# Performance work log

Measured on AMD Instinct MI355X. Metric: run time of the kernel, lower is better.

Reference implementation:

```python
import jax, jax.numpy as jnp
import numpy as np
import math

CHANNELS = 512
OUT_CHANNELS = 512
N_HEADS = 8
WINDOW = 4
K_CH = CHANNELS // N_HEADS


def _conv1x1(x, W, b):
    # x: (B, C_in, T), W: (C_out, C_in), b: (C_out,)
    return jnp.einsum('oc,bct->bot', W, x) + b[None, :, None]


def _get_relative_embeddings(emb, length, window=WINDOW):
    # emb: (H, 2*window+1, k_ch) -> (H, 2*length-1, k_ch)
    pad_length = max(length - (window + 1), 0)
    start = max(window + 1 - length, 0)
    e = jnp.pad(emb, ((0, 0), (pad_length, pad_length), (0, 0))) if pad_length > 0 else emb
    return e[:, start:start + 2 * length - 1]


def _relative_to_absolute(x):
    # x: (B, H, L, 2L-1) -> (B, H, L, L)
    b, h, L, _ = x.shape
    x = jnp.pad(x, ((0, 0), (0, 0), (0, 0), (0, 1)))          # (B,H,L,2L)
    xf = x.reshape(b, h, L * 2 * L)
    xf = jnp.pad(xf, ((0, 0), (0, 0), (L - 1, 0)))
    return xf.reshape(b, h, L + 1, 2 * L - 1)[:, :, :L, L - 1:]


def _absolute_to_relative(x):
    # x: (B, H, L, L) -> (B, H, L, 2L-1)
    b, h, L, _ = x.shape
    x = jnp.pad(x, ((0, 0), (0, 0), (0, 0), (0, L - 1)))       # (B,H,L,2L-1)
    xf = x.reshape(b, h, L * (2 * L - 1))
    xf = jnp.pad(xf, ((0, 0), (0, 0), (L, 0)))
    return xf.reshape(b, h, L, 2 * L)[:, :, :, 1:]


def setup_inputs() -> dict:
    key = jax.random.key(0)
    ks = jax.random.split(key, 16)
    B, C, T = 4, CHANNELS, 1024
    xavier = math.sqrt(2.0 / (C + C))
    rel_std = K_CH ** -0.5
    return {
        'x_q': jax.random.normal(ks[0], (B, C, T), jnp.float32),
        'x_k': jax.random.normal(ks[1], (B, C, T), jnp.float32),
        'x_v': jax.random.normal(ks[2], (B, C, T), jnp.float32),
        'Wq': jax.random.normal(ks[3], (C, C), jnp.float32) * xavier,
        'bq': jnp.zeros((C,), jnp.float32),
        'Wk': jax.random.normal(ks[4], (C, C), jnp.float32) * xavier,
        'bk': jnp.zeros((C,), jnp.float32),
        'Wv': jax.random.normal(ks[5], (C, C), jnp.float32) * xavier,
        'bv': jnp.zeros((C,), jnp.float32),
        'Wo': jax.random.normal(ks[6], (OUT_CHANNELS, C), jnp.float32) * xavier,
        'bo': jnp.zeros((OUT_CHANNELS,), jnp.float32),
        'emb_rel_k': jax.random.normal(ks[7], (N_HEADS, 2 * WINDOW + 1, K_CH), jnp.float32) * rel_std,
        'emb_rel_v': jax.random.normal(ks[8], (N_HEADS, 2 * WINDOW + 1, K_CH), jnp.float32) * rel_std,
    }


def reference(x_q, x_k, x_v, Wq, bq, Wk, bk, Wv, bv, Wo, bo, emb_rel_k, emb_rel_v):
    q = _conv1x1(x_q, Wq, bq)
    k = _conv1x1(x_k, Wk, bk)
    v = _conv1x1(x_v, Wv, bv)
    B, C, T = q.shape
    # (B, C, T) -> (B, H, T, k_ch); head h owns contiguous k_ch channel chunk
    qh = q.reshape(B, N_HEADS, K_CH, T).transpose(0, 1, 3, 2) / math.sqrt(K_CH)
    kh = k.reshape(B, N_HEADS, K_CH, T).transpose(0, 1, 3, 2)
    vh = v.reshape(B, N_HEADS, K_CH, T).transpose(0, 1, 3, 2)
    scores = jnp.einsum('bhtd,bhsd->bhts', qh, kh)              # (B,H,T,T)
    rel_k = _get_relative_embeddings(emb_rel_k, T)              # (H,2T-1,d)
    rel_logits = jnp.einsum('bhtd,hmd->bhtm', qh, rel_k)        # (B,H,T,2T-1)
    scores = scores + _relative_to_absolute(rel_logits)
    attn = jax.nn.softmax(scores, axis=-1)
    ctx = jnp.einsum('bhts,bhsd->bhtd', attn, vh)
    rel_w = _absolute_to_relative(attn)                         # (B,H,T,2T-1)
    rel_v = _get_relative_embeddings(emb_rel_v, T)
    ctx = ctx + jnp.einsum('bhtm,hmd->bhtd', rel_w, rel_v)
    out = ctx.transpose(0, 1, 3, 2).reshape(B, C, T)
    return _conv1x1(out, Wo, bo)
```

## Files before the change

### kernel.cpp

```cpp
#include <hip/hip_runtime.h>

#define T_LEN 1024
#define NH 8
#define DH 64
#define CCH 512
#define LOG2E 1.44269504088896340736f

typedef _Float16 f16;
typedef _Float16 f16x8 __attribute__((ext_vector_type(8)));
typedef _Float16 f16x4 __attribute__((ext_vector_type(4)));
typedef float f32x4 __attribute__((ext_vector_type(4)));

__device__ __forceinline__ void dma16(const void* g, void* l)
{
    __builtin_amdgcn_global_load_lds((const __attribute__((address_space(1))) void*)g,
                                     (__attribute__((address_space(3))) void*)l, 16, 0, 0);
}

__global__ __launch_bounds__(256)
void prep_kernel(const float* __restrict__ x0, const float* __restrict__ x1,
                 const float* __restrict__ x2, const float* __restrict__ W0,
                 const float* __restrict__ W1, const float* __restrict__ W2,
                 const float* __restrict__ W3, f16* __restrict__ o0,
                 f16* __restrict__ o1, f16* __restrict__ o2, f16* __restrict__ w0,
                 f16* __restrict__ w1, f16* __restrict__ w2, f16* __restrict__ w3,
                 int B)
{
    const int z = blockIdx.z;
    if (z < 3 * B) {
        const int t0 = blockIdx.x * 64, c0 = blockIdx.y * 64;
        const int which = z / B, b = z % B;
        const float* x = (which == 0) ? x0 : (which == 1) ? x1 : x2;
        f16* o = (which == 0) ? o0 : (which == 1) ? o1 : o2;

        __shared__ float L[64 * 68];
        const int cl = threadIdx.x & 63, g = threadIdx.x >> 6;
        const float* src = x + ((size_t)(b * CCH + c0 + cl)) * T_LEN + t0 + g * 16;
        #pragma unroll
        for (int j = 0; j < 4; ++j)
            *(float4*)&L[cl * 68 + g * 16 + 4 * j] = *(const float4*)&src[4 * j];
        __syncthreads();
        const int tl = threadIdx.x & 63, cg = (threadIdx.x >> 6) * 16;
        f16 h[16];
        #pragma unroll
        for (int j = 0; j < 16; ++j) h[j] = (f16)L[(cg + j) * 68 + tl];
        f16* dst = o + ((size_t)(b * T_LEN + t0 + tl)) * CCH + c0 + cg;
        *(f16x8*)&dst[0] = *(f16x8*)&h[0];
        *(f16x8*)&dst[8] = *(f16x8*)&h[8];
    } else {
        const int slice = z - 3 * B;
        size_t i = ((size_t)(slice * 128 + blockIdx.y * 16 + blockIdx.x) * 256 + threadIdx.x) * 4;
        const int wi = (int)(i >> 18);
        const size_t off = i & 262143;
        const float* src = (wi == 0) ? W0 : (wi == 1) ? W1 : (wi == 2) ? W2 : W3;
        f16* dst = (wi == 0) ? w0 : (wi == 1) ? w1 : (wi == 2) ? w2 : w3;
        float4 v4 = *(const float4*)&src[off];
        f16x4 h = {(f16)v4.x, (f16)v4.y, (f16)v4.z, (f16)v4.w};
        *(f16x4*)&dst[off] = h;
    }
}

__global__ __launch_bounds__(256)
void proj_qkv(const f16* __restrict__ xq, const f16* __restrict__ xk,
              const f16* __restrict__ xv, const f16* __restrict__ wq,
              const f16* __restrict__ wk, const f16* __restrict__ wv,
              const float* __restrict__ bq, const float* __restrict__ bk,
              const float* __restrict__ bv, f16* __restrict__ qo,
              f16* __restrict__ ko, f16* __restrict__ vo)
{
    const int which = blockIdx.z;
    const f16* X = (which == 0) ? xq : (which == 1) ? xk : xv;
    const f16* W = (which == 0) ? wq : (which == 1) ? wk : wv;
    const float* bias = (which == 0) ? bq : (which == 1) ? bk : bv;
    const float scale = (which == 0) ? 0.125f * LOG2E : 1.0f;

    const int r0 = blockIdx.x * 128;
    const int o0 = blockIdx.y * 64;
    const int tid = threadIdx.x;
    const int w = tid >> 6, lane = tid & 63;
    const int quad = lane >> 4, l15 = lane & 15;

    __shared__ __align__(16) f16 Xs[2][128 * 64];
    __shared__ __align__(16) f16 Ws[2][64 * 64];

    const int srow = tid >> 3;
    const int scol = ((tid & 7) ^ (srow & 7)) << 3;

    const f16* Xg = X + (size_t)(r0 + srow) * CCH + scol;
    const f16* Wg = W + (size_t)(o0 + srow) * CCH + scol;

    #pragma unroll
    for (int j = 0; j < 4; ++j)
        dma16(Xg + (size_t)(32 * j) * CCH, &Xs[0][(size_t)tid * 8 + j * 2048]);
    #pragma unroll
    for (int j = 0; j < 2; ++j)
        dma16(Wg + (size_t)(32 * j) * CCH, &Ws[0][(size_t)tid * 8 + j * 2048]);

    f32x4 acc[8] = {};

    for (int kc = 0; kc < 8; ++kc) {
        __syncthreads();
        if (kc < 7) {
            const int bf = (kc + 1) & 1, c1 = (kc + 1) * 64;
            #pragma unroll
            for (int j = 0; j < 4; ++j)
                dma16(Xg + c1 + (size_t)(32 * j) * CCH, &Xs[bf][(size_t)tid * 8 + j * 2048]);
            #pragma unroll
            for (int j = 0; j < 2; ++j)
                dma16(Wg + c1 + (size_t)(32 * j) * CCH, &Ws[bf][(size_t)tid * 8 + j * 2048]);
        }
        const int cb = kc & 1;
        #pragma unroll
        for (int ks = 0; ks < 2; ++ks) {
            const int sl = ((ks * 4 + quad) ^ (l15 & 7)) << 3;
            f16x8 xf[2], wf[4];
            #pragma unroll
            for (int im = 0; im < 2; ++im)
                xf[im] = *(const f16x8*)&Xs[cb][(32 * w + 16 * im + l15) * 64 + sl];
            #pragma unroll
            for (int cm = 0; cm < 4; ++cm)
                wf[cm] = *(const f16x8*)&Ws[cb][(16 * cm + l15) * 64 + sl];
            if (which < 2) {
                #pragma unroll
                for (int im = 0; im < 2; ++im)
                    #pragma unroll
                    for (int cm = 0; cm < 4; ++cm)
                        acc[im * 4 + cm] = __builtin_amdgcn_mfma_f32_16x16x32_f16(
                            xf[im], wf[cm], acc[im * 4 + cm], 0, 0, 0);
            } else {
                #pragma unroll
                for (int cm = 0; cm < 4; ++cm)
                    #pragma unroll
                    for (int in = 0; in < 2; ++in)
                        acc[cm * 2 + in] = __builtin_amdgcn_mfma_f32_16x16x32_f16(
                            wf[cm], xf[in], acc[cm * 2 + in], 0, 0, 0);
            }
        }
    }

    if (which < 2) {
        f16* out = (which == 0) ? qo : ko;
        float bl[4];
        #pragma unroll
        for (int cm = 0; cm < 4; ++cm) bl[cm] = bias[o0 + 16 * cm + l15];
        #pragma unroll
        for (int im = 0; im < 2; ++im)
            #pragma unroll
            for (int r = 0; r < 4; ++r) {
                size_t row = (size_t)(r0 + 32 * w + 16 * im + 4 * quad + r) * CCH;
                #pragma unroll
                for (int cm = 0; cm < 4; ++cm)
                    out[row + o0 + 16 * cm + l15] =
                        (f16)((acc[im * 4 + cm][r] + bl[cm]) * scale);
            }
    } else {
        const int bb = r0 >> 10, tb = r0 & 1023;
        #pragma unroll
        for (int cm = 0; cm < 4; ++cm) {
            float4 bv4 = *(const float4*)&bias[o0 + 16 * cm + 4 * quad];
            float bl[4] = {bv4.x, bv4.y, bv4.z, bv4.w};
            #pragma unroll
            for (int r = 0; r < 4; ++r) {
                size_t row = ((size_t)(bb * CCH + o0 + 16 * cm + 4 * quad + r)) * T_LEN;
                #pragma unroll
                for (int in = 0; in < 2; ++in)
                    vo[row + tb + 32 * w + 16 * in + l15] =
                        (f16)(acc[cm * 2 + in][r] + bl[r]);
            }
        }
    }
}

__global__ __launch_bounds__(256)
void attn_mfma(const f16* __restrict__ q, const f16* __restrict__ kk,
               const f16* __restrict__ v, const float* __restrict__ ekg,
               const float* __restrict__ evg, f16* __restrict__ Op0,
               f16* __restrict__ Op1, float* __restrict__ l0,
               float* __restrict__ l1)
{
    const int t0 = blockIdx.x * 64, h = blockIdx.y;
    const int b = blockIdx.z >> 1, split = blockIdx.z & 1;
    const int tid = threadIdx.x;
    const int w = tid >> 6, lane = tid & 63;
    const int quad = lane >> 4, l15 = lane & 15;

    f16* Op = split ? Op1 : Op0;
    float* lbuf = split ? l1 : l0;

    __shared__ __align__(16) f16 Qs[4096], Ks[4096], Vs[4096], Ps[4096];
    __shared__ float eks[576], evs[576];

    const int srow = tid >> 3;
    const int scol = ((tid & 7) ^ (srow & 7)) << 3;

    for (int i = tid; i < 576; i += 256) {
        eks[i] = ekg[h * 576 + i];
        evs[i] = evg[h * 576 + i];
    }

    dma16(q + ((size_t)(b * T_LEN + t0 + srow)) * CCH + h * DH + scol, &Qs[(size_t)tid * 8]);
    dma16(q + ((size_t)(b * T_LEN + t0 + srow + 32)) * CCH + h * DH + scol, &Qs[((size_t)tid + 256) * 8]);
    __syncthreads();

    f16x8 qf[2];
    #pragma unroll
    for (int ks = 0; ks < 2; ++ks)
        qf[ks] = *(const f16x8*)&Qs[(16 * w + l15) * 64 + (((ks * 4 + quad) ^ (l15 & 7)) << 3)];

    const int kb0 = split * 8;
    const f16* gk = kk + ((size_t)(b * T_LEN + kb0 * 64 + srow)) * CCH + h * DH + scol;
    const f16* gv = v + ((size_t)(b * CCH + h * DH + srow)) * T_LEN + kb0 * 64 + scol;

    const int myt = 16 * w + l15;
    float Ssum = 0.f;
    f32x4 O[4] = {};

    const bool corner_hi = (blockIdx.x == 0) && (split == 1);
    const bool corner_lo = (blockIdx.x == 15) && (split == 0);

    for (int kb = kb0; kb < kb0 + 8; ++kb) {
        __syncthreads();
        dma16(gk, &Ks[(size_t)tid * 8]);
        dma16(gk + (size_t)32 * CCH, &Ks[((size_t)tid + 256) * 8]);
        dma16(gv, &Vs[(size_t)tid * 8]);
        dma16(gv + (size_t)32 * T_LEN, &Vs[((size_t)tid + 256) * 8]);
        gk += (size_t)64 * CCH;
        gv += 64;
        __syncthreads();

        f32x4 S[4] = {};
        #pragma unroll
        for (int ks = 0; ks < 2; ++ks) {
            #pragma unroll
            for (int ct = 0; ct < 4; ++ct) {
                f16x8 a = *(const f16x8*)&Ks[(16 * ct + l15) * 64 + (((ks * 4 + quad) ^ (l15 & 7)) << 3)];
                S[ct] = __builtin_amdgcn_mfma_f32_16x16x32_f16(a, qf[ks], S[ct], 0, 0, 0);
            }
        }

        if ((corner_hi && kb == 15) || (corner_lo && kb == 0)) {
            const int s0g = kb * 64;
            #pragma unroll
            for (int ct = 0; ct < 4; ++ct)
                #pragma unroll
                for (int r = 0; r < 4; ++r) {
                    int t_g = t0 + myt;
                    int s_g = s0g + 16 * ct + 4 * quad + r;
                    int df = s_g - t_g;
                    if (df >= 1019 && df <= 1023) {
                        const float* ekp = &eks[(df - 1019) * 64];
                        float sacc = 0.f;
                        for (int d = 0; d < 64; ++d)
                            sacc += (float)Qs[myt * 64 + (((d >> 3) ^ (myt & 7)) << 3) + (d & 7)] * ekp[d];
                        S[ct][r] += sacc;
                    } else if (df >= -1023 && df <= -1021) {
                        const float* ekp = &eks[(1029 + df) * 64];
                        const int t2 = myt - 1;
                        float sacc = 0.f;
                        for (int d = 0; d < 64; ++d)
                            sacc += (float)Qs[t2 * 64 + (((d >> 3) ^ (t2 & 7)) << 3) + (d & 7)] * ekp[d];
                        S[ct][r] += sacc;
                    }
                }
        }

        #pragma unroll
        for (int ct = 0; ct < 4; ++ct) {
            f16x4 pk_;
            #pragma unroll
            for (int r = 0; r < 4; ++r) {
                float p = exp2f(S[ct][r]);
                Ssum += p;
                pk_[r] = (f16)p;
            }
            int colh = (((2 * ct + (quad >> 1)) ^ (myt & 7)) << 3) + (quad & 1) * 4;
            *(f16x4*)&Ps[myt * 64 + colh] = pk_;
        }
        __syncthreads();

        #pragma unroll
        for (int ks = 0; ks < 2; ++ks) {
            f16x8 a = *(const f16x8*)&Ps[(16 * w + l15) * 64 + (((ks * 4 + quad) ^ (l15 & 7)) << 3)];
            #pragma unroll
            for (int ct = 0; ct < 4; ++ct) {
                f16x8 bf = *(const f16x8*)&Vs[(16 * ct + l15) * 64 + (((ks * 4 + quad) ^ (l15 & 7)) << 3)];
                O[ct] = __builtin_amdgcn_mfma_f32_16x16x32_f16(a, bf, O[ct], 0, 0, 0);
            }
        }

        const int s0g = kb * 64;
        if (s0g <= t0 + 67 && s0g + 63 >= t0 - 4) {
            #pragma unroll
            for (int r = 0; r < 4; ++r) {
                int t_loc = 16 * w + 4 * quad + r;
                int t_g = t0 + t_loc;
                int slo = max(s0g, t_g - 4), shi = min(s0g + 63, t_g + 4);
                for (int s = slo; s <= shi; ++s) {
                    int sl = s - s0g;
                    float p = (float)Ps[t_loc * 64 + (((sl >> 3) ^ (t_loc & 7)) << 3) + (sl & 7)];
                    const float* evp = &evs[(s - t_g + 4) * 64];
                    #pragma unroll
                    for (int ct = 0; ct < 4; ++ct)
                        O[ct][r] += p * evp[16 * ct + l15];
                }
            }
        }
    }

    Ssum += __shfl_xor(Ssum, 16);
    Ssum += __shfl_xor(Ssum, 32);
    if (quad == 0)
        lbuf[((size_t)b * NH + h) * T_LEN + t0 + myt] = Ssum;

    #pragma unroll
    for (int r = 0; r < 4; ++r) {
        int t_g = t0 + 16 * w + 4 * quad + r;
        size_t rowo = ((size_t)(b * T_LEN + t_g)) * CCH + h * DH;
        #pragma unroll
        for (int ct = 0; ct < 4; ++ct)
            Op[rowo + 16 * ct + l15] = (f16)O[ct][r];
    }
}

__global__ __launch_bounds__(256)
void combine_kernel(const f16* __restrict__ Op0, const f16* __restrict__ Op1,
                    const float* __restrict__ l0, const float* __restrict__ l1,
                    f16* __restrict__ ctx)
{
    const size_t i8 = ((size_t)blockIdx.x * 256 + threadIdx.x) * 8;
    const size_t gr = i8 >> 9;
    const int h = (int)((i8 & 511) >> 6);
    const size_t li = ((gr >> 10) * NH + h) * T_LEN + (gr & 1023);
    const float rl = 1.0f / (l0[li] + l1[li]);
    f16x8 a0 = *(const f16x8*)&Op0[i8];
    f16x8 a1 = *(const f16x8*)&Op1[i8];
    f16 o[8];
    #pragma unroll
    for (int e = 0; e < 8; ++e)
        o[e] = (f16)(((float)a0[e] + (float)a1[e]) * rl);
    *(f16x8*)&ctx[i8] = *(f16x8*)o;
}

__global__ __launch_bounds__(256)
void proj_out(const f16* __restrict__ ctx, const f16* __restrict__ Wo,
              const float* __restrict__ bo, float* __restrict__ out)
{
    const int r0 = blockIdx.x * 128;
    const int o0 = blockIdx.y * 64;
    const int tid = threadIdx.x;
    const int w = tid >> 6, lane = tid & 63;
    const int quad = lane >> 4, l15 = lane & 15;

    __shared__ __align__(16) f16 Cs[2][128 * 64];
    __shared__ __align__(16) f16 Ws[2][64 * 64];

    const int srow = tid >> 3;
    const int scol = ((tid & 7) ^ (srow & 7)) << 3;

    const f16* Cg = ctx + (size_t)(r0 + srow) * CCH + scol;
    const f16* Wg = Wo + (size_t)(o0 + srow) * CCH + scol;

    #pragma unroll
    for (int j = 0; j < 4; ++j)
        dma16(Cg + (size_t)(32 * j) * CCH, &Cs[0][(size_t)tid * 8 + j * 2048]);
    #pragma unroll
    for (int j = 0; j < 2; ++j)
        dma16(Wg + (size_t)(32 * j) * CCH, &Ws[0][(size_t)tid * 8 + j * 2048]);

    f32x4 acc[8] = {};

    for (int kc = 0; kc < 8; ++kc) {
        __syncthreads();
        if (kc < 7) {
            const int bf = (kc + 1) & 1, c1 = (kc + 1) * 64;
            #pragma unroll
            for (int j = 0; j < 4; ++j)
                dma16(Cg + c1 + (size_t)(32 * j) * CCH, &Cs[bf][(size_t)tid * 8 + j * 2048]);
            #pragma unroll
            for (int j = 0; j < 2; ++j)
                dma16(Wg + c1 + (size_t)(32 * j) * CCH, &Ws[bf][(size_t)tid * 8 + j * 2048]);
        }
        const int cb = kc & 1;
        #pragma unroll
        for (int ks = 0; ks < 2; ++ks) {
            const int sl = ((ks * 4 + quad) ^ (l15 & 7)) << 3;
            f16x8 cf[2], wf[4];
            #pragma unroll
            for (int in = 0; in < 2; ++in)
                cf[in] = *(const f16x8*)&Cs[cb][(32 * w + 16 * in + l15) * 64 + sl];
            #pragma unroll
            for (int cm = 0; cm < 4; ++cm)
                wf[cm] = *(const f16x8*)&Ws[cb][(16 * cm + l15) * 64 + sl];
            #pragma unroll
            for (int cm = 0; cm < 4; ++cm)
                #pragma unroll
                for (int in = 0; in < 2; ++in)
                    acc[cm * 2 + in] = __builtin_amdgcn_mfma_f32_16x16x32_f16(
                        wf[cm], cf[in], acc[cm * 2 + in], 0, 0, 0);
        }
    }

    const int bb = r0 >> 10, tb = r0 & 1023;
    #pragma unroll
    for (int cm = 0; cm < 4; ++cm) {
        float4 bv4 = *(const float4*)&bo[o0 + 16 * cm + 4 * quad];
        float bl[4] = {bv4.x, bv4.y, bv4.z, bv4.w};
        #pragma unroll
        for (int r = 0; r < 4; ++r) {
            size_t row = ((size_t)(bb * CCH + o0 + 16 * cm + 4 * quad + r)) * T_LEN;
            #pragma unroll
            for (int in = 0; in < 2; ++in)
                out[row + tb + 32 * w + 16 * in + l15] = acc[cm * 2 + in][r] + bl[r];
        }
    }
}

extern "C" void kernel_launch(void* const* d_in, const int* in_sizes, int n_in,
                              void* d_out, int out_size, void* d_ws, size_t ws_size,
                              hipStream_t stream)
{
    const float* x_q = (const float*)d_in[0];
    const float* x_k = (const float*)d_in[1];
    const float* x_v = (const float*)d_in[2];
    const float* Wq  = (const float*)d_in[3];
    const float* bq  = (const float*)d_in[4];
    const float* Wk  = (const float*)d_in[5];
    const float* bk  = (const float*)d_in[6];
    const float* Wv  = (const float*)d_in[7];
    const float* bv  = (const float*)d_in[8];
    const float* Wo  = (const float*)d_in[9];
    const float* bo  = (const float*)d_in[10];
    const float* erk = (const float*)d_in[11];
    const float* erv = (const float*)d_in[12];

    const int B = in_sizes[0] / (CCH * T_LEN);
    const size_t te = (size_t)B * CCH * T_LEN;
    const size_t we = (size_t)CCH * CCH;

    f16* p = (f16*)d_ws;
    f16* xTq = p; p += te;
    f16* xTk = p; p += te;
    f16* xTv = p; p += te;
    f16* wqh = p; p += we;
    f16* wkh = p; p += we;
    f16* wvh = p; p += we;
    f16* woh = p; p += we;
    f16* qh  = p; p += te;
    f16* kh  = p; p += te;
    f16* vh  = p; p += te;
    f16* Op0 = p; p += te;
    f16* Op1 = p; p += te;
    f16* ch  = p; p += te;
    float* l0 = (float*)p;
    float* l1 = l0 + (size_t)B * NH * T_LEN;

    dim3 blk(256);
    prep_kernel<<<dim3(16, 8, 3 * B + 8), blk, 0, stream>>>(
        x_q, x_k, x_v, Wq, Wk, Wv, Wo, xTq, xTk, xTv, wqh, wkh, wvh, woh, B);
    proj_qkv<<<dim3(B * 8, 8, 3), blk, 0, stream>>>(
        xTq, xTk, xTv, wqh, wkh, wvh, bq, bk, bv, qh, kh, vh);
    attn_mfma<<<dim3(T_LEN / 64, NH, 2 * B), blk, 0, stream>>>(
        qh, kh, vh, erk, erv, Op0, Op1, l0, l1);
    combine_kernel<<<dim3(B * 256), blk, 0, stream>>>(Op0, Op1, l0, l1, ch);
    proj_out<<<dim3(B * 8, 8), blk, 0, stream>>>(ch, woh, bo, (float*)d_out);
}
```

Before: 159.8 us.

## Load unshared MFMA operands directly from global memory instead of LDS

In the QKV projection, attention and output projection kernels, operand tiles that each wave uses alone (X rows, K and V tiles, context rows) are no longer staged through shared memory. Each lane now reads its MFMA fragment straight from global memory, which removes DMA copies, LDS traffic and two barriers per key block in attention. The output projection also halves its row tile to 64 so there are twice as many blocks. The cost is uncoalesced 16-byte global reads that depend on cache hits, and K/V loads that are no longer prefetched.

```diff
diff --git a/kernel.cpp b/kernel.cpp
--- a/kernel.cpp
+++ b/kernel.cpp
@@ -80,18 +80,14 @@
     const int w = tid >> 6, lane = tid & 63;
     const int quad = lane >> 4, l15 = lane & 15;
 
-    __shared__ __align__(16) f16 Xs[2][128 * 64];
     __shared__ __align__(16) f16 Ws[2][64 * 64];
 
     const int srow = tid >> 3;
     const int scol = ((tid & 7) ^ (srow & 7)) << 3;
-
-    const f16* Xg = X + (size_t)(r0 + srow) * CCH + scol;
     const f16* Wg = W + (size_t)(o0 + srow) * CCH + scol;
 
-    #pragma unroll
-    for (int j = 0; j < 4; ++j)
-        dma16(Xg + (size_t)(32 * j) * CCH, &Xs[0][(size_t)tid * 8 + j * 2048]);
+    const f16* xp = X + (size_t)(r0 + 32 * w + l15) * CCH + quad * 8;
+
     #pragma unroll
     for (int j = 0; j < 2; ++j)
         dma16(Wg + (size_t)(32 * j) * CCH, &Ws[0][(size_t)tid * 8 + j * 2048]);
@@ -103,9 +99,6 @@
         if (kc < 7) {
             const int bf = (kc + 1) & 1, c1 = (kc + 1) * 64;
             #pragma unroll
-            for (int j = 0; j < 4; ++j)
-                dma16(Xg + c1 + (size_t)(32 * j) * CCH, &Xs[bf][(size_t)tid * 8 + j * 2048]);
-            #pragma unroll
             for (int j = 0; j < 2; ++j)
                 dma16(Wg + c1 + (size_t)(32 * j) * CCH, &Ws[bf][(size_t)tid * 8 + j * 2048]);
         }
@@ -116,7 +109,7 @@
             f16x8 xf[2], wf[4];
             #pragma unroll
             for (int im = 0; im < 2; ++im)
-                xf[im] = *(const f16x8*)&Xs[cb][(32 * w + 16 * im + l15) * 64 + sl];
+                xf[im] = *(const f16x8*)&xp[(size_t)(16 * im) * CCH + kc * 64 + ks * 32];
             #pragma unroll
             for (int cm = 0; cm < 4; ++cm)
                 wf[cm] = *(const f16x8*)&Ws[cb][(16 * cm + l15) * 64 + sl];
@@ -187,7 +180,7 @@
     f16* Op = split ? Op1 : Op0;
     float* lbuf = split ? l1 : l0;
 
-    __shared__ __align__(16) f16 Qs[4096], Ks[4096], Vs[4096], Ps[4096];
+    __shared__ __align__(16) f16 Qs[4096], Ps[4096];
     __shared__ float eks[576], evs[576];
 
     const int srow = tid >> 3;
@@ -208,8 +201,8 @@
         qf[ks] = *(const f16x8*)&Qs[(16 * w + l15) * 64 + (((ks * 4 + quad) ^ (l15 & 7)) << 3)];
 
     const int kb0 = split * 8;
-    const f16* gk = kk + ((size_t)(b * T_LEN + kb0 * 64 + srow)) * CCH + h * DH + scol;
-    const f16* gv = v + ((size_t)(b * CCH + h * DH + srow)) * T_LEN + kb0 * 64 + scol;
+    const f16* kp = kk + ((size_t)(b * T_LEN + kb0 * 64 + l15)) * CCH + h * DH + quad * 8;
+    const f16* vp = v + ((size_t)(b * CCH + h * DH + l15)) * T_LEN + kb0 * 64 + quad * 8;
 
     const int myt = 16 * w + l15;
     float Ssum = 0.f;
@@ -219,23 +212,18 @@
     const bool corner_lo = (blockIdx.x == 15) && (split == 0);
 
     for (int kb = kb0; kb < kb0 + 8; ++kb) {
-        __syncthreads();
-        dma16(gk, &Ks[(size_t)tid * 8]);
-        dma16(gk + (size_t)32 * CCH, &Ks[((size_t)tid + 256) * 8]);
-        dma16(gv, &Vs[(size_t)tid * 8]);
-        dma16(gv + (size_t)32 * T_LEN, &Vs[((size_t)tid + 256) * 8]);
-        gk += (size_t)64 * CCH;
-        gv += 64;
-        __syncthreads();
+        const int ko = (kb - kb0) * 64;
 
         f32x4 S[4] = {};
         #pragma unroll
         for (int ks = 0; ks < 2; ++ks) {
-            #pragma unroll
-            for (int ct = 0; ct < 4; ++ct) {
-                f16x8 a = *(const f16x8*)&Ks[(16 * ct + l15) * 64 + (((ks * 4 + quad) ^ (l15 & 7)) << 3)];
-                S[ct] = __builtin_amdgcn_mfma_f32_16x16x32_f16(a, qf[ks], S[ct], 0, 0, 0);
-            }
+            f16x8 kf[4];
+            #pragma unroll
+            for (int ct = 0; ct < 4; ++ct)
+                kf[ct] = *(const f16x8*)&kp[(size_t)(ko + 16 * ct) * CCH + ks * 32];
+            #pragma unroll
+            for (int ct = 0; ct < 4; ++ct)
+                S[ct] = __builtin_amdgcn_mfma_f32_16x16x32_f16(kf[ct], qf[ks], S[ct], 0, 0, 0);
         }
 
         if ((corner_hi && kb == 15) || (corner_lo && kb == 0)) {
@@ -264,28 +252,34 @@
                 }
         }
 
-        #pragma unroll
-        for (int ct = 0; ct < 4; ++ct) {
-            f16x4 pk_;
+        f16x4 pk_[4];
+        #pragma unroll
+        for (int ct = 0; ct < 4; ++ct)
             #pragma unroll
             for (int r = 0; r < 4; ++r) {
                 float p = exp2f(S[ct][r]);
                 Ssum += p;
-                pk_[r] = (f16)p;
-            }
+                pk_[ct][r] = (f16)p;
+            }
+
+        __syncthreads();
+        #pragma unroll
+        for (int ct = 0; ct < 4; ++ct) {
             int colh = (((2 * ct + (quad >> 1)) ^ (myt & 7)) << 3) + (quad & 1) * 4;
-            *(f16x4*)&Ps[myt * 64 + colh] = pk_;
+            *(f16x4*)&Ps[myt * 64 + colh] = pk_[ct];
         }
         __syncthreads();
 
         #pragma unroll
         for (int ks = 0; ks < 2; ++ks) {
             f16x8 a = *(const f16x8*)&Ps[(16 * w + l15) * 64 + (((ks * 4 + quad) ^ (l15 & 7)) << 3)];
-            #pragma unroll
-            for (int ct = 0; ct < 4; ++ct) {
-                f16x8 bf = *(const f16x8*)&Vs[(16 * ct + l15) * 64 + (((ks * 4 + quad) ^ (l15 & 7)) << 3)];
-                O[ct] = __builtin_amdgcn_mfma_f32_16x16x32_f16(a, bf, O[ct], 0, 0, 0);
-            }
+            f16x8 vf[4];
+            #pragma unroll
+            for (int ct = 0; ct < 4; ++ct)
+                vf[ct] = *(const f16x8*)&vp[(size_t)(16 * ct) * T_LEN + ko + ks * 32];
+            #pragma unroll
+            for (int ct = 0; ct < 4; ++ct)
+                O[ct] = __builtin_amdgcn_mfma_f32_16x16x32_f16(a, vf[ct], O[ct], 0, 0, 0);
         }
 
         const int s0g = kb * 64;
@@ -345,38 +339,31 @@
 void proj_out(const f16* __restrict__ ctx, const f16* __restrict__ Wo,
               const float* __restrict__ bo, float* __restrict__ out)
 {
-    const int r0 = blockIdx.x * 128;
+    const int r0 = blockIdx.x * 64;
     const int o0 = blockIdx.y * 64;
     const int tid = threadIdx.x;
     const int w = tid >> 6, lane = tid & 63;
     const int quad = lane >> 4, l15 = lane & 15;
 
-    __shared__ __align__(16) f16 Cs[2][128 * 64];
     __shared__ __align__(16) f16 Ws[2][64 * 64];
 
     const int srow = tid >> 3;
     const int scol = ((tid & 7) ^ (srow & 7)) << 3;
-
-    const f16* Cg = ctx + (size_t)(r0 + srow) * CCH + scol;
     const f16* Wg = Wo + (size_t)(o0 + srow) * CCH + scol;
 
-    #pragma unroll
-    for (int j = 0; j < 4; ++j)
-        dma16(Cg + (size_t)(32 * j) * CCH, &Cs[0][(size_t)tid * 8 + j * 2048]);
+    const f16* cp = ctx + (size_t)(r0 + 16 * w + l15) * CCH + quad * 8;
+
     #pragma unroll
     for (int j = 0; j < 2; ++j)
         dma16(Wg + (size_t)(32 * j) * CCH, &Ws[0][(size_t)tid * 8 + j * 2048]);
 
-    f32x4 acc[8] = {};
+    f32x4 acc[4] = {};
 
     for (int kc = 0; kc < 8; ++kc) {
         __syncthreads();
         if (kc < 7) {
             const int bf = (kc + 1) & 1, c1 = (kc + 1) * 64;
             #pragma unroll
-            for (int j = 0; j < 4; ++j)
-                dma16(Cg + c1 + (size_t)(32 * j) * CCH, &Cs[bf][(size_t)tid * 8 + j * 2048]);
-            #pragma unroll
             for (int j = 0; j < 2; ++j)
                 dma16(Wg + c1 + (size_t)(32 * j) * CCH, &Ws[bf][(size_t)tid * 8 + j * 2048]);
         }
@@ -384,19 +371,12 @@
         #pragma unroll
         for (int ks = 0; ks < 2; ++ks) {
             const int sl = ((ks * 4 + quad) ^ (l15 & 7)) << 3;
-            f16x8 cf[2], wf[4];
-            #pragma unroll
-            for (int in = 0; in < 2; ++in)
-                cf[in] = *(const f16x8*)&Cs[cb][(32 * w + 16 * in + l15) * 64 + sl];
-            #pragma unroll
-            for (int cm = 0; cm < 4; ++cm)
-                wf[cm] = *(const f16x8*)&Ws[cb][(16 * cm + l15) * 64 + sl];
-            #pragma unroll
-            for (int cm = 0; cm < 4; ++cm)
-                #pragma unroll
-                for (int in = 0; in < 2; ++in)
-                    acc[cm * 2 + in] = __builtin_amdgcn_mfma_f32_16x16x32_f16(
-                        wf[cm], cf[in], acc[cm * 2 + in], 0, 0, 0);
+            f16x8 cf = *(const f16x8*)&cp[kc * 64 + ks * 32];
+            #pragma unroll
+            for (int cm = 0; cm < 4; ++cm) {
+                f16x8 wf = *(const f16x8*)&Ws[cb][(16 * cm + l15) * 64 + sl];
+                acc[cm] = __builtin_amdgcn_mfma_f32_16x16x32_f16(wf, cf, acc[cm], 0, 0, 0);
+            }
         }
     }
 
@@ -408,9 +388,7 @@
         #pragma unroll
         for (int r = 0; r < 4; ++r) {
             size_t row = ((size_t)(bb * CCH + o0 + 16 * cm + 4 * quad + r)) * T_LEN;
-            #pragma unroll
-            for (int in = 0; in < 2; ++in)
-                out[row + tb + 32 * w + 16 * in + l15] = acc[cm * 2 + in][r] + bl[r];
+            out[row + tb + 16 * w + l15] = acc[cm][r] + bl[r];
         }
     }
 }
@@ -462,5 +440,5 @@
     attn_mfma<<<dim3(T_LEN / 64, NH, 2 * B), blk, 0, stream>>>(
         qh, kh, vh, erk, erv, Op0, Op1, l0, l1);
     combine_kernel<<<dim3(B * 256), blk, 0, stream>>>(Op0, Op1, l0, l1, ch);
-    proj_out<<<dim3(B * 8, 8), blk, 0, stream>>>(ch, woh, bo, (float*)d_out);
-}
+    proj_out<<<dim3(B * 16, 8), blk, 0, stream>>>(ch, woh, bo, (float*)d_out);
+}
```

After: 213.4 us. +33.5%, slower.

## Double-buffer K/V tiles in attention and fuse split-combine into output projection

Applied to the files above, without the earlier changes.

The attention kernel now keeps two K/V shared-memory buffers and issues the next tile's loads after the softmax barrier, so they overlap with the PV MFMA work instead of stalling at the top of each iteration. The separate combine kernel is removed. Its normalization of the two split partial outputs moves into proj_out's tile loading, which reads both partials, scales by the reciprocal row sums from shared memory, and writes f16 into LDS. This saves a launch and the ctx round trip through memory. In exchange, proj_out uses register-staged loads instead of async LDS DMA and rereads the partials once per output-column block, and the attention kernel uses more LDS.

```diff
diff --git a/kernel.cpp b/kernel.cpp
--- a/kernel.cpp
+++ b/kernel.cpp
@@ -187,7 +187,8 @@
     f16* Op = split ? Op1 : Op0;
     float* lbuf = split ? l1 : l0;
 
-    __shared__ __align__(16) f16 Qs[4096], Ks[4096], Vs[4096], Ps[4096];
+    __shared__ __align__(16) f16 Qs[4096], Ps[4096];
+    __shared__ __align__(16) f16 Ks[2][4096], Vs[2][4096];
     __shared__ float eks[576], evs[576];
 
     const int srow = tid >> 3;
@@ -198,19 +199,23 @@
         evs[i] = evg[h * 576 + i];
     }
 
-    dma16(q + ((size_t)(b * T_LEN + t0 + srow)) * CCH + h * DH + scol, &Qs[(size_t)tid * 8]);
-    dma16(q + ((size_t)(b * T_LEN + t0 + srow + 32)) * CCH + h * DH + scol, &Qs[((size_t)tid + 256) * 8]);
-    __syncthreads();
-
-    f16x8 qf[2];
-    #pragma unroll
-    for (int ks = 0; ks < 2; ++ks)
-        qf[ks] = *(const f16x8*)&Qs[(16 * w + l15) * 64 + (((ks * 4 + quad) ^ (l15 & 7)) << 3)];
-
     const int kb0 = split * 8;
     const f16* gk = kk + ((size_t)(b * T_LEN + kb0 * 64 + srow)) * CCH + h * DH + scol;
     const f16* gv = v + ((size_t)(b * CCH + h * DH + srow)) * T_LEN + kb0 * 64 + scol;
 
+    dma16(q + ((size_t)(b * T_LEN + t0 + srow)) * CCH + h * DH + scol, &Qs[(size_t)tid * 8]);
+    dma16(q + ((size_t)(b * T_LEN + t0 + srow + 32)) * CCH + h * DH + scol, &Qs[((size_t)tid + 256) * 8]);
+    dma16(gk, &Ks[0][(size_t)tid * 8]);
+    dma16(gk + (size_t)32 * CCH, &Ks[0][((size_t)tid + 256) * 8]);
+    dma16(gv, &Vs[0][(size_t)tid * 8]);
+    dma16(gv + (size_t)32 * T_LEN, &Vs[0][((size_t)tid + 256) * 8]);
+    __syncthreads();
+
+    f16x8 qf[2];
+    #pragma unroll
+    for (int ks = 0; ks < 2; ++ks)
+        qf[ks] = *(const f16x8*)&Qs[(16 * w + l15) * 64 + (((ks * 4 + quad) ^ (l15 & 7)) << 3)];
+
     const int myt = 16 * w + l15;
     float Ssum = 0.f;
     f32x4 O[4] = {};
@@ -218,22 +223,16 @@
     const bool corner_hi = (blockIdx.x == 0) && (split == 1);
     const bool corner_lo = (blockIdx.x == 15) && (split == 0);
 
-    for (int kb = kb0; kb < kb0 + 8; ++kb) {
-        __syncthreads();
-        dma16(gk, &Ks[(size_t)tid * 8]);
-        dma16(gk + (size_t)32 * CCH, &Ks[((size_t)tid + 256) * 8]);
-        dma16(gv, &Vs[(size_t)tid * 8]);
-        dma16(gv + (size_t)32 * T_LEN, &Vs[((size_t)tid + 256) * 8]);
-        gk += (size_t)64 * CCH;
-        gv += 64;
-        __syncthreads();
+    for (int it = 0; it < 8; ++it) {
+        const int kb = kb0 + it, cb = it & 1;
+        if (it) __syncthreads();
 
         f32x4 S[4] = {};
         #pragma unroll
         for (int ks = 0; ks < 2; ++ks) {
             #pragma unroll
             for (int ct = 0; ct < 4; ++ct) {
-                f16x8 a = *(const f16x8*)&Ks[(16 * ct + l15) * 64 + (((ks * 4 + quad) ^ (l15 & 7)) << 3)];
+                f16x8 a = *(const f16x8*)&Ks[cb][(16 * ct + l15) * 64 + (((ks * 4 + quad) ^ (l15 & 7)) << 3)];
                 S[ct] = __builtin_amdgcn_mfma_f32_16x16x32_f16(a, qf[ks], S[ct], 0, 0, 0);
             }
         }
@@ -278,12 +277,20 @@
         }
         __syncthreads();
 
+        if (it < 7) {
+            const int nb = cb ^ 1;
+            dma16(gk + (size_t)((it + 1) * 64) * CCH, &Ks[nb][(size_t)tid * 8]);
+            dma16(gk + (size_t)((it + 1) * 64 + 32) * CCH, &Ks[nb][((size_t)tid + 256) * 8]);
+            dma16(gv + (it + 1) * 64, &Vs[nb][(size_t)tid * 8]);
+            dma16(gv + (size_t)32 * T_LEN + (it + 1) * 64, &Vs[nb][((size_t)tid + 256) * 8]);
+        }
+
         #pragma unroll
         for (int ks = 0; ks < 2; ++ks) {
             f16x8 a = *(const f16x8*)&Ps[(16 * w + l15) * 64 + (((ks * 4 + quad) ^ (l15 & 7)) << 3)];
             #pragma unroll
             for (int ct = 0; ct < 4; ++ct) {
-                f16x8 bf = *(const f16x8*)&Vs[(16 * ct + l15) * 64 + (((ks * 4 + quad) ^ (l15 & 7)) << 3)];
+                f16x8 bf = *(const f16x8*)&Vs[cb][(16 * ct + l15) * 64 + (((ks * 4 + quad) ^ (l15 & 7)) << 3)];
                 O[ct] = __builtin_amdgcn_mfma_f32_16x16x32_f16(a, bf, O[ct], 0, 0, 0);
             }
         }
@@ -323,27 +330,10 @@
 }
 
 __global__ __launch_bounds__(256)
-void combine_kernel(const f16* __restrict__ Op0, const f16* __restrict__ Op1,
-                    const float* __restrict__ l0, const float* __restrict__ l1,
-                    f16* __restrict__ ctx)
-{
-    const size_t i8 = ((size_t)blockIdx.x * 256 + threadIdx.x) * 8;
-    const size_t gr = i8 >> 9;
-    const int h = (int)((i8 & 511) >> 6);
-    const size_t li = ((gr >> 10) * NH + h) * T_LEN + (gr & 1023);
-    const float rl = 1.0f / (l0[li] + l1[li]);
-    f16x8 a0 = *(const f16x8*)&Op0[i8];
-    f16x8 a1 = *(const f16x8*)&Op1[i8];
-    f16 o[8];
-    #pragma unroll
-    for (int e = 0; e < 8; ++e)
-        o[e] = (f16)(((float)a0[e] + (float)a1[e]) * rl);
-    *(f16x8*)&ctx[i8] = *(f16x8*)o;
-}
-
-__global__ __launch_bounds__(256)
-void proj_out(const f16* __restrict__ ctx, const f16* __restrict__ Wo,
-              const float* __restrict__ bo, float* __restrict__ out)
+void proj_out(const f16* __restrict__ Op0, const f16* __restrict__ Op1,
+              const float* __restrict__ l0, const float* __restrict__ l1,
+              const f16* __restrict__ Wo, const float* __restrict__ bo,
+              float* __restrict__ out)
 {
     const int r0 = blockIdx.x * 128;
     const int o0 = blockIdx.y * 64;
@@ -353,19 +343,38 @@
 
     __shared__ __align__(16) f16 Cs[2][128 * 64];
     __shared__ __align__(16) f16 Ws[2][64 * 64];
+    __shared__ float rls[128 * 8];
 
     const int srow = tid >> 3;
-    const int scol = ((tid & 7) ^ (srow & 7)) << 3;
-
-    const f16* Cg = ctx + (size_t)(r0 + srow) * CCH + scol;
+    const int slot = tid & 7;
+    const int scol = (slot ^ (srow & 7)) << 3;
+
+    for (int idx = tid; idx < 1024; idx += 256) {
+        int row = idx >> 3, hh = idx & 7;
+        size_t gr = r0 + row;
+        size_t li = ((gr >> 10) * NH + hh) * T_LEN + (gr & 1023);
+        rls[idx] = 1.0f / (l0[li] + l1[li]);
+    }
+    __syncthreads();
+
     const f16* Wg = Wo + (size_t)(o0 + srow) * CCH + scol;
 
-    #pragma unroll
-    for (int j = 0; j < 4; ++j)
-        dma16(Cg + (size_t)(32 * j) * CCH, &Cs[0][(size_t)tid * 8 + j * 2048]);
     #pragma unroll
     for (int j = 0; j < 2; ++j)
         dma16(Wg + (size_t)(32 * j) * CCH, &Ws[0][(size_t)tid * 8 + j * 2048]);
+    #pragma unroll
+    for (int j = 0; j < 4; ++j) {
+        int row = srow + 32 * j;
+        size_t src = (size_t)(r0 + row) * CCH + scol;
+        f16x8 a0 = *(const f16x8*)&Op0[src];
+        f16x8 a1 = *(const f16x8*)&Op1[src];
+        float rl = rls[row * 8];
+        f16 hx[8];
+        #pragma unroll
+        for (int e = 0; e < 8; ++e)
+            hx[e] = (f16)(((float)a0[e] + (float)a1[e]) * rl);
+        *(f16x8*)&Cs[0][row * 64 + slot * 8] = *(f16x8*)hx;
+    }
 
     f32x4 acc[8] = {};
 
@@ -374,11 +383,21 @@
         if (kc < 7) {
             const int bf = (kc + 1) & 1, c1 = (kc + 1) * 64;
             #pragma unroll
-            for (int j = 0; j < 4; ++j)
-                dma16(Cg + c1 + (size_t)(32 * j) * CCH, &Cs[bf][(size_t)tid * 8 + j * 2048]);
-            #pragma unroll
             for (int j = 0; j < 2; ++j)
                 dma16(Wg + c1 + (size_t)(32 * j) * CCH, &Ws[bf][(size_t)tid * 8 + j * 2048]);
+            #pragma unroll
+            for (int j = 0; j < 4; ++j) {
+                int row = srow + 32 * j;
+                size_t src = (size_t)(r0 + row) * CCH + c1 + scol;
+                f16x8 a0 = *(const f16x8*)&Op0[src];
+                f16x8 a1 = *(const f16x8*)&Op1[src];
+                float rl = rls[row * 8 + kc + 1];
+                f16 hx[8];
+                #pragma unroll
+                for (int e = 0; e < 8; ++e)
+                    hx[e] = (f16)(((float)a0[e] + (float)a1[e]) * rl);
+                *(f16x8*)&Cs[bf][row * 64 + slot * 8] = *(f16x8*)hx;
+            }
         }
         const int cb = kc & 1;
         #pragma unroll
@@ -450,7 +469,6 @@
     f16* vh  = p; p += te;
     f16* Op0 = p; p += te;
     f16* Op1 = p; p += te;
-    f16* ch  = p; p += te;
     float* l0 = (float*)p;
     float* l1 = l0 + (size_t)B * NH * T_LEN;
 
@@ -461,6 +479,6 @@
         xTq, xTk, xTv, wqh, wkh, wvh, bq, bk, bv, qh, kh, vh);
     attn_mfma<<<dim3(T_LEN / 64, NH, 2 * B), blk, 0, stream>>>(
         qh, kh, vh, erk, erv, Op0, Op1, l0, l1);
-    combine_kernel<<<dim3(B * 256), blk, 0, stream>>>(Op0, Op1, l0, l1, ch);
-    proj_out<<<dim3(B * 8, 8), blk, 0, stream>>>(ch, woh, bo, (float*)d_out);
-}
+    proj_out<<<dim3(B * 8, 8), blk, 0, stream>>>(
+        Op0, Op1, l0, l1, woh, bo, (float*)d_out);
+}
```

Measured after the change: 158.4 us. About the same (-0.8%).
